# Performance work log

Measured on AMD Instinct MI355X. Metric: run time of the kernel, lower is better.

The kernel has to match this reference:

```python
import jax, jax.numpy as jnp
import numpy as np

B, N, CIN, COUT = 8192, 17, 256, 256


def setup_inputs() -> dict:
    key = jax.random.key(0)
    k_x, k_w, k_m, k_a, k_b = jax.random.split(key, 5)
    stdv = 1.0 / np.sqrt(COUT)
    return {
        "x": jax.random.normal(k_x, (B, N, CIN), dtype=jnp.float32),
        # xavier_uniform with gain=1.414 ~ U(-a, a), a = gain*sqrt(6/(fan_in+fan_out))
        "W": jax.random.uniform(k_w, (2, CIN, COUT), dtype=jnp.float32,
                                minval=-1.0, maxval=1.0) * (1.414 * np.sqrt(6.0 / (CIN + COUT))),
        # M initialized to ones in torch; perturb slightly to exercise the math
        "M": 1.0 + 0.1 * jax.random.normal(k_m, (N, COUT), dtype=jnp.float32),
        "adj": jax.random.uniform(k_a, (N, N), dtype=jnp.float32),
        "adj2": jnp.full((N, N), 1e-6, dtype=jnp.float32),
        "bias": jax.random.uniform(k_b, (COUT,), dtype=jnp.float32,
                                   minval=-stdv, maxval=stdv),
    }


def reference(x, W, M, adj, adj2, bias):
    # x: [B, N, Cin], W: [2, Cin, Cout], M: [N, Cout], adj/adj2: [N, N]
    h0 = jnp.einsum("bnc,cd->bnd", x, W[0])  # [B, N, Cout]
    h1 = jnp.einsum("bnc,cd->bnd", x, W[1])  # [B, N, Cout]
    A = adj + adj2
    A = (A.T + A) * 0.5                       # symmetrize
    E = jnp.eye(A.shape[0], dtype=x.dtype)
    out = (jnp.einsum("ij,bjd->bid", A * E, M * h0)
           + jnp.einsum("ij,bjd->bid", A * (1.0 - E), M * h1))
    return out + bias[None, None, :]
```

## Files before the change

kernel.cpp:

```cpp
#include <hip/hip_runtime.h>
#include <hip/hip_bf16.h>

typedef float  f32x4  __attribute__((ext_vector_type(4)));
typedef __bf16 bf16x8 __attribute__((ext_vector_type(8)));
typedef short  s16x8  __attribute__((ext_vector_type(8)));
typedef short  s16x4  __attribute__((ext_vector_type(4)));

__device__ __forceinline__ short f2b(float f) {
  unsigned u = __builtin_bit_cast(unsigned, f);
  u = (u + 0x7fffu + ((u >> 16) & 1u)) >> 16;
  return (short)u;
}
__device__ __forceinline__ float b2f(short s) {
  unsigned u = ((unsigned)(unsigned short)s) << 16;
  return __builtin_bit_cast(float, u);
}
__device__ __forceinline__ s16x4 pack4(f32x4 a) {
  union { s16x4 v; __hip_bfloat162 h[2]; } u;
  u.h[0] = __float22bfloat162_rn(make_float2(a[0], a[1]));
  u.h[1] = __float22bfloat162_rn(make_float2(a[2], a[3]));
  return u.v;
}

__global__ void prep_wt(const float* __restrict__ W, short* __restrict__ Wt) {
  int q = blockIdx.x * blockDim.x + threadIdx.x;
  int mat = q >> 14;
  int rem = q & 16383;
  int d   = rem >> 6;
  int c4  = (rem & 63) << 2;
  const float* src = W + mat * 65536;
  s16x4 o;
  #pragma unroll
  for (int i = 0; i < 4; ++i) o[i] = f2b(src[(c4 + i) * 256 + d]);
  *(s16x4*)&Wt[q << 2] = o;
}

__global__ __launch_bounds__(256)
void fused_mgc(const float* __restrict__ x, const short* __restrict__ Wt,
               const float* __restrict__ M, const float* __restrict__ adj,
               const float* __restrict__ adj2, const float* __restrict__ bias,
               float* __restrict__ out) {
  __shared__ short xs[8976];
  __shared__ float ms[2176];
  __shared__ float aoff[289];
  __shared__ float diagl[17];

  const int tid  = threadIdx.x;
  const int lane = tid & 63;
  const int wv   = tid >> 6;
  const int m16  = lane & 15;
  const int qd   = lane >> 4;

  const int phys   = blockIdx.x;
  const int xcd    = phys & 7;
  const int iseq   = phys >> 3;
  const int ct     = iseq & 1;
  const int btbase = (xcd * 64 + (iseq >> 1)) * 8;

  const int c4 = (tid & 63) << 2;
  const int r0 = tid >> 6;

  f32x4 xp[9];
  {
    const float* xb = x + (size_t)btbase * 34 * 256;
    #pragma unroll
    for (int it = 0; it < 9; ++it) {
      int row = r0 + it * 4;
      if (row < 34) xp[it] = *(const f32x4*)&xb[row * 256 + c4];
    }
  }
  for (int idx = tid; idx < 289; idx += 256) {
    int i = idx / 17, j = idx - i * 17;
    float v = 0.5f * ((adj[i*17+j] + adj2[i*17+j]) + (adj[j*17+i] + adj2[j*17+i]));
    aoff[idx] = (i == j) ? 0.0f : v;
    if (i == j) diagl[i] = adj[i*17+i] + adj2[i*17+i];
  }
  for (int q = tid; q < 544; q += 256) {
    int n = q >> 5, cq = (q & 31) << 2;
    *(f32x4*)&ms[n * 128 + cq] = *(const f32x4*)&M[n * 256 + ct * 128 + cq];
  }

  const short* wbase = Wt + (ct * 128 + wv * 32 + m16) * 256;

  int arow[3];
  #pragma unroll
  for (int rf = 0; rf < 3; ++rf) {
    int r = rf * 16 + m16;
    arow[rf] = (r < 34 ? r : 33) * 264;
  }

  const int d7   = tid & 127;
  const int g    = tid >> 7;
  const float bi = bias[ct * 128 + d7];

  for (int t = 0; t < 8; ++t) {
    const int bt = btbase + t;

    #pragma unroll
    for (int it = 0; it < 9; ++it) {
      int row = r0 + it * 4;
      if (row < 34) *(s16x4*)&xs[row * 264 + c4] = pack4(xp[it]);
    }
    __syncthreads();

    if (t < 7) {
      const float* xb = x + (size_t)(bt + 1) * 34 * 256;
      #pragma unroll
      for (int it = 0; it < 9; ++it) {
        int row = r0 + it * 4;
        if (row < 34) xp[it] = *(const f32x4*)&xb[row * 256 + c4];
      }
    }

    f32x4 acc[3][4];
    #pragma unroll
    for (int a = 0; a < 3; ++a)
      #pragma unroll
      for (int b = 0; b < 4; ++b) acc[a][b] = (f32x4)0.0f;

    #pragma unroll
    for (int ks = 0; ks < 8; ++ks) {
      const int kq = ks * 32 + qd * 8;
      bf16x8 bfr[4];
      #pragma unroll
      for (int mc = 0; mc < 4; ++mc) {
        int mat = mc >> 1, cf = mc & 1;
        s16x8 w = *(const s16x8*)&wbase[mat * 65536 + cf * 4096 + kq];
        bfr[mc] = __builtin_bit_cast(bf16x8, w);
      }
      #pragma unroll
      for (int rf = 0; rf < 3; ++rf) {
        s16x8 a8 = *(const s16x8*)&xs[arow[rf] + kq];
        bf16x8 af = __builtin_bit_cast(bf16x8, a8);
        #pragma unroll
        for (int mc = 0; mc < 4; ++mc)
          acc[rf][mc] = __builtin_amdgcn_mfma_f32_16x16x32_bf16(af, bfr[mc], acc[rf][mc], 0, 0, 0);
      }
    }
    __syncthreads();

    short* sbuf = xs;
    short* gbuf = xs + 4488;
    #pragma unroll
    for (int rf = 0; rf < 3; ++rf) {
      #pragma unroll
      for (int cf = 0; cf < 2; ++cf) {
        int c = wv * 32 + cf * 16 + m16;
        #pragma unroll
        for (int reg = 0; reg < 4; ++reg) {
          int r = rf * 16 + qd * 4 + reg;
          if (r < 34) {
            int n = r - (r >= 17 ? 17 : 0);
            float mv = ms[n * 128 + c];
            sbuf[r * 132 + c] = f2b(diagl[n] * mv * acc[rf][cf][reg]);
            gbuf[r * 132 + c] = f2b(mv * acc[rf][2 + cf][reg]);
          }
        }
      }
    }
    __syncthreads();

    {
      int rbase = g * 17;
      float gr[17];
      #pragma unroll
      for (int j = 0; j < 17; ++j) gr[j] = b2f(gbuf[(rbase + j) * 132 + d7]);
      #pragma unroll
      for (int i = 0; i < 17; ++i) {
        float s = b2f(sbuf[(rbase + i) * 132 + d7]) + bi;
        #pragma unroll
        for (int j = 0; j < 17; ++j) s += aoff[i * 17 + j] * gr[j];
        out[((bt * 2 + g) * 17 + i) * 256 + ct * 128 + d7] = s;
      }
    }
    __syncthreads();
  }
}

extern "C" void kernel_launch(void* const* d_in, const int* in_sizes, int n_in,
                              void* d_out, int out_size, void* d_ws, size_t ws_size,
                              hipStream_t stream) {
  const float* x    = (const float*)d_in[0];
  const float* W    = (const float*)d_in[1];
  const float* M    = (const float*)d_in[2];
  const float* adj  = (const float*)d_in[3];
  const float* adj2 = (const float*)d_in[4];
  const float* bias = (const float*)d_in[5];
  float* out = (float*)d_out;
  short* Wt  = (short*)d_ws;

  prep_wt<<<128, 256, 0, stream>>>(W, Wt);
  fused_mgc<<<1024, 256, 0, stream>>>(x, Wt, M, adj, adj2, bias, out);
}
```

Before: 366.3 us.

## Double-buffer x tiles in LDS, halve per-block batches, split mixing accumulators

Each block now keeps two x staging buffers plus dedicated sbuf/gbuf arrays. The next tile is packed into the alternate buffer during the epilogue, which removes two of the four barriers per iteration. The grid is doubled to 2048 blocks with 4 batch tiles each instead of 8, giving more parallelism and a shorter tail. The 17-term adjacency mix now uses four independent accumulators to shorten the FMA dependency chain. LDS use per block roughly doubles, which may lower occupancy.

```diff
diff --git a/kernel.cpp b/kernel.cpp
--- a/kernel.cpp
+++ b/kernel.cpp
@@ -40,7 +40,10 @@
                const float* __restrict__ M, const float* __restrict__ adj,
                const float* __restrict__ adj2, const float* __restrict__ bias,
                float* __restrict__ out) {
-  __shared__ short xs[8976];
+  __shared__ short xs0[8976];
+  __shared__ short xs1[8976];
+  __shared__ short sbuf[4488];
+  __shared__ short gbuf[4488];
   __shared__ float ms[2176];
   __shared__ float aoff[289];
   __shared__ float diagl[17];
@@ -55,7 +58,7 @@
   const int xcd    = phys & 7;
   const int iseq   = phys >> 3;
   const int ct     = iseq & 1;
-  const int btbase = (xcd * 64 + (iseq >> 1)) * 8;
+  const int btbase = (xcd * 128 + (iseq >> 1)) * 4;
 
   const int c4 = (tid & 63) << 2;
   const int r0 = tid >> 6;
@@ -79,6 +82,11 @@
     int n = q >> 5, cq = (q & 31) << 2;
     *(f32x4*)&ms[n * 128 + cq] = *(const f32x4*)&M[n * 256 + ct * 128 + cq];
   }
+  #pragma unroll
+  for (int it = 0; it < 9; ++it) {
+    int row = r0 + it * 4;
+    if (row < 34) *(s16x4*)&xs0[row * 264 + c4] = pack4(xp[it]);
+  }
 
   const short* wbase = Wt + (ct * 128 + wv * 32 + m16) * 256;
 
@@ -93,17 +101,15 @@
   const int g    = tid >> 7;
   const float bi = bias[ct * 128 + d7];
 
-  for (int t = 0; t < 8; ++t) {
+  __syncthreads();
+
+  const short* xsp = xs0;
+  short*       xsn = xs1;
+
+  for (int t = 0; t < 4; ++t) {
     const int bt = btbase + t;
 
-    #pragma unroll
-    for (int it = 0; it < 9; ++it) {
-      int row = r0 + it * 4;
-      if (row < 34) *(s16x4*)&xs[row * 264 + c4] = pack4(xp[it]);
-    }
-    __syncthreads();
-
-    if (t < 7) {
+    if (t < 3) {
       const float* xb = x + (size_t)(bt + 1) * 34 * 256;
       #pragma unroll
       for (int it = 0; it < 9; ++it) {
@@ -130,17 +136,14 @@
       }
       #pragma unroll
       for (int rf = 0; rf < 3; ++rf) {
-        s16x8 a8 = *(const s16x8*)&xs[arow[rf] + kq];
+        s16x8 a8 = *(const s16x8*)&xsp[arow[rf] + kq];
         bf16x8 af = __builtin_bit_cast(bf16x8, a8);
         #pragma unroll
         for (int mc = 0; mc < 4; ++mc)
           acc[rf][mc] = __builtin_amdgcn_mfma_f32_16x16x32_bf16(af, bfr[mc], acc[rf][mc], 0, 0, 0);
       }
     }
-    __syncthreads();
-
-    short* sbuf = xs;
-    short* gbuf = xs + 4488;
+
     #pragma unroll
     for (int rf = 0; rf < 3; ++rf) {
       #pragma unroll
@@ -158,6 +161,15 @@
         }
       }
     }
+
+    if (t < 3) {
+      #pragma unroll
+      for (int it = 0; it < 9; ++it) {
+        int row = r0 + it * 4;
+        if (row < 34) *(s16x4*)&xsn[row * 264 + c4] = pack4(xp[it]);
+      }
+    }
+
     __syncthreads();
 
     {
@@ -167,13 +179,27 @@
       for (int j = 0; j < 17; ++j) gr[j] = b2f(gbuf[(rbase + j) * 132 + d7]);
       #pragma unroll
       for (int i = 0; i < 17; ++i) {
-        float s = b2f(sbuf[(rbase + i) * 132 + d7]) + bi;
+        const float* ar = &aoff[i * 17];
+        float s0 = ar[0] * gr[0] + b2f(sbuf[(rbase + i) * 132 + d7]) + bi;
+        float s1 = ar[1] * gr[1];
+        float s2 = ar[2] * gr[2];
+        float s3 = ar[3] * gr[3];
         #pragma unroll
-        for (int j = 0; j < 17; ++j) s += aoff[i * 17 + j] * gr[j];
-        out[((bt * 2 + g) * 17 + i) * 256 + ct * 128 + d7] = s;
-      }
-    }
+        for (int j = 4; j < 16; j += 4) {
+          s0 += ar[j]     * gr[j];
+          s1 += ar[j + 1] * gr[j + 1];
+          s2 += ar[j + 2] * gr[j + 2];
+          s3 += ar[j + 3] * gr[j + 3];
+        }
+        s0 += ar[16] * gr[16];
+        out[((size_t)(bt * 2 + g) * 17 + i) * 256 + ct * 128 + d7] =
+            (s0 + s1) + (s2 + s3);
+      }
+    }
+
     __syncthreads();
+
+    const short* tmp = xsp; xsp = xsn; xsn = (short*)tmp;
   }
 }
 
@@ -190,5 +216,5 @@
   short* Wt  = (short*)d_ws;
 
   prep_wt<<<128, 256, 0, stream>>>(W, Wt);
-  fused_mgc<<<1024, 256, 0, stream>>>(x, Wt, M, adj, adj2, bias, out);
-}
+  fused_mgc<<<2048, 256, 0, stream>>>(x, Wt, M, adj, adj2, bias, out);
+}
```

Measured after the change: 408.5 us. +11.5%, slower.
